# Performance work log

Measured on AMD Instinct MI355X. Metric: run time of the kernel, lower is better.

## Reference

```python
import jax, jax.numpy as jnp
import numpy as np

NUM_CLASSES = 19
EPS_MEAN = 1e-6   # torch: denominator eps in per-class mean
EPS_COS = 1e-8    # torch CosineSimilarity default eps


def _nearest_resize_labels(target, H, W):
    # torch nn.Upsample(mode='nearest'): in_idx = floor(out_idx * in / out)
    th, tw = target.shape[1], target.shape[2]
    ih = (jnp.arange(H) * th) // H
    iw = (jnp.arange(W) * tw) // W
    return target[:, ih][:, :, iw]  # [B,H,W]


def _class_centers(feat, lab):
    # feat: [B,C,H,W]; lab: [B,H,W] int. Single-pass segment mean by class,
    # then scatter means back to pixels whose label is in [0, NUM_CLASSES).
    B, C, H, W = feat.shape
    f = feat.reshape(B, C, H * W)                 # [B,C,N]
    l = lab.reshape(B, H * W)                      # [B,N]
    onehot = jax.nn.one_hot(l, NUM_CLASSES, dtype=feat.dtype)  # [B,N,K]; out-of-range -> all-zero row
    sums = jnp.einsum('bcn,bnk->bck', f, onehot)   # per-class channel sums
    counts = onehot.sum(axis=1)                    # [B,K]
    means = sums / (counts[:, None, :] + EPS_MEAN) # [B,C,K]
    gathered = jnp.einsum('bck,bnk->bcn', means, onehot)  # mean at each valid pixel, 0 elsewhere
    valid = (l >= 0) & (l < NUM_CLASSES)           # [B,N]
    center = jnp.where(valid[:, None, :], gathered, f)
    return center.reshape(B, C, H, W)


def _cosine_dim1(a, b):
    # torch CosineSimilarity(dim=1): dot / (max(||a||,eps) * max(||b||,eps))
    num = (a * b).sum(axis=1)
    na = jnp.sqrt((a * a).sum(axis=1))
    nb = jnp.sqrt((b * b).sum(axis=1))
    return num / (jnp.maximum(na, EPS_COS) * jnp.maximum(nb, EPS_COS))


def setup_inputs() -> dict:
    key = jax.random.key(0)
    k1, k2, k3 = jax.random.split(key, 3)
    B, C, H, W = 8, 512, 64, 64
    preds_S = jax.random.normal(k1, (B, C, H, W), dtype=jnp.float32)
    preds_T = jax.random.normal(k2, (B, C, H, W), dtype=jnp.float32)
    target = jax.random.randint(k3, (B, 512, 512), 0, NUM_CLASSES, dtype=jnp.int64)
    return {"preds_S": preds_S, "preds_T": preds_T, "target": target}


def reference(preds_S, preds_T, target):
    H, W = preds_S.shape[2], preds_S.shape[3]
    lab = _nearest_resize_labels(target, H, W)     # [B,H,W]
    center_S = _class_centers(preds_S, lab)
    center_T = _class_centers(preds_T, lab)
    pcsim_S = _cosine_dim1(preds_S, center_S)      # [B,H,W]
    pcsim_T = _cosine_dim1(preds_T, center_T)
    return jnp.mean((pcsim_S - pcsim_T) ** 2)
```

## Files before the change

kernel.cpp:

```cpp
#include <hip/hip_runtime.h>

#define NCLS   19
#define NB     8
#define NC     512
#define NHW    4096
#define EPSM   1e-6f
#define EPSC   1e-8f

#define OFF_LABELS   0u
#define OFF_COUNTS   131072u
#define OFF_SUMS_S   132096u
#define OFF_SUMS_T   443392u
#define OFF_NORM_S   754688u
#define OFF_NORM_T   755712u
#define OFF_PART     756736u

template<int CTRL>
__device__ __forceinline__ float dpp_add(float x) {
    int y = __builtin_amdgcn_update_dpp(0, __float_as_int(x), CTRL, 0xf, 0xf, false);
    return x + __int_as_float(y);
}
__device__ __forceinline__ float wave64_sum(float x) {
    x = dpp_add<0x111>(x);
    x = dpp_add<0x112>(x);
    x = dpp_add<0x114>(x);
    x = dpp_add<0x118>(x);
    x = dpp_add<0x142>(x);
    x = dpp_add<0x143>(x);
    return x;
}

__global__ __launch_bounds__(256) void k_labels(const int* __restrict__ target,
                                                int* __restrict__ labels,
                                                float* __restrict__ counts) {
    __shared__ int hist[NCLS];
    const int b = blockIdx.x;
    const int t = threadIdx.x;
    if (t < NCLS) hist[t] = 0;
    __syncthreads();
    const int* tb = target + (size_t)b * 512 * 512;
    #pragma unroll
    for (int i = 0; i < 16; ++i) {
        int n = t + i * 256;
        int y = n >> 6, x = n & 63;
        int l = tb[(y * 8) * 512 + x * 8];
        labels[b * NHW + n] = l;
        if (l >= 0 && l < NCLS) atomicAdd(&hist[l], 1);
    }
    __syncthreads();
    if (t < NCLS) counts[b * NCLS + t] = (float)hist[t];
}

__global__ __launch_bounds__(256, 2) void k_sums(const float* __restrict__ fS,
                                                 const float* __restrict__ fT,
                                                 const int* __restrict__ labels,
                                                 float* __restrict__ sumsS,
                                                 float* __restrict__ sumsT) {
    const int t = threadIdx.x;
    const int lane = t & 63;
    const int u = (blockIdx.x << 2) + (t >> 6);
    const int b = u >> 8;
    const int c0 = (u & 255) << 1;
    const size_t base = ((size_t)(b * NC) + c0) * NHW;
    const float4* pS0 = (const float4*)(fS + base);
    const float4* pS1 = (const float4*)(fS + base + NHW);
    const float4* pT0 = (const float4*)(fT + base);
    const float4* pT1 = (const float4*)(fT + base + NHW);
    const int4* lab4 = (const int4*)(labels + b * NHW);

    float aS0[NCLS], aS1[NCLS], aT0[NCLS], aT1[NCLS];
    #pragma unroll
    for (int k = 0; k < NCLS; ++k) { aS0[k] = aS1[k] = aT0[k] = aT1[k] = 0.f; }

    #pragma unroll 2
    for (int i = 0; i < 16; ++i) {
        const int idx = lane + (i << 6);
        const float4 vS0 = pS0[idx];
        const float4 vS1 = pS1[idx];
        const float4 vT0 = pT0[idx];
        const float4 vT1 = pT1[idx];
        const int4 l4 = lab4[idx];
        #pragma unroll
        for (int k = 0; k < NCLS; ++k) {
            const float m0 = (l4.x == k) ? 1.f : 0.f;
            const float m1 = (l4.y == k) ? 1.f : 0.f;
            const float m2 = (l4.z == k) ? 1.f : 0.f;
            const float m3 = (l4.w == k) ? 1.f : 0.f;
            aS0[k] += m0 * vS0.x + m1 * vS0.y + m2 * vS0.z + m3 * vS0.w;
            aS1[k] += m0 * vS1.x + m1 * vS1.y + m2 * vS1.z + m3 * vS1.w;
            aT0[k] += m0 * vT0.x + m1 * vT0.y + m2 * vT0.z + m3 * vT0.w;
            aT1[k] += m0 * vT1.x + m1 * vT1.y + m2 * vT1.z + m3 * vT1.w;
        }
    }
    #pragma unroll
    for (int k = 0; k < NCLS; ++k) {
        aS0[k] = wave64_sum(aS0[k]);
        aS1[k] = wave64_sum(aS1[k]);
        aT0[k] = wave64_sum(aT0[k]);
        aT1[k] = wave64_sum(aT1[k]);
    }
    if (lane == 63) {
        #pragma unroll
        for (int k = 0; k < NCLS; ++k) {
            float2* dS = (float2*)(sumsS + ((size_t)(b * NCLS + k)) * NC + c0);
            float2* dT = (float2*)(sumsT + ((size_t)(b * NCLS + k)) * NC + c0);
            *dS = make_float2(aS0[k], aS1[k]);
            *dT = make_float2(aT0[k], aT1[k]);
        }
    }
}

__global__ __launch_bounds__(64) void k_means(float* __restrict__ sumsS,
                                              float* __restrict__ sumsT,
                                              const float* __restrict__ counts,
                                              float* __restrict__ normS,
                                              float* __restrict__ normT) {
    const int bk = blockIdx.x;
    const int t = threadIdx.x;
    const float inv = 1.f / (counts[bk] + EPSM);
    float* rS = sumsS + (size_t)bk * NC;
    float* rT = sumsT + (size_t)bk * NC;
    float aS = 0.f, aT = 0.f;
    #pragma unroll
    for (int i = 0; i < NC / 64; ++i) {
        float mS = rS[t + i * 64] * inv; rS[t + i * 64] = mS; aS += mS * mS;
        float mT = rT[t + i * 64] * inv; rT[t + i * 64] = mT; aT += mT * mT;
    }
    aS = wave64_sum(aS);
    aT = wave64_sum(aT);
    if (t == 63) { normS[bk] = sqrtf(aS); normT[bk] = sqrtf(aT); }
}

#define CCH 64
__global__ __launch_bounds__(256) void k_dots(const float* __restrict__ fS,
                                              const float* __restrict__ fT,
                                              const float* __restrict__ meansS,
                                              const float* __restrict__ meansT,
                                              const int* __restrict__ labels,
                                              float* __restrict__ part) {
    __shared__ float mS[NCLS * 65];
    __shared__ float mT[NCLS * 65];
    const int blk = blockIdx.x;
    const int chunk = blk & 7;
    const int tile  = (blk >> 3) & 15;
    const int b     = blk >> 7;
    const int t = threadIdx.x;
    const int c0 = chunk * CCH;
    const int n = tile * 256 + t;

    for (int i = t; i < NCLS * CCH; i += 256) {
        const int k = i >> 6, j = i & 63;
        mS[k * 65 + j] = meansS[((size_t)(b * NCLS + k)) * NC + c0 + j];
        mT[k * 65 + j] = meansT[((size_t)(b * NCLS + k)) * NC + c0 + j];
    }
    __syncthreads();

    const int l = labels[b * NHW + n];
    const int lc = (l >= 0 && l < NCLS) ? l : 0;
    const float* pS = fS + ((size_t)(b * NC + c0)) * NHW + n;
    const float* pT = fT + ((size_t)(b * NC + c0)) * NHW + n;
    float dS = 0.f, nS = 0.f, dT = 0.f, nT = 0.f;
    #pragma unroll 8
    for (int ci = 0; ci < CCH; ++ci) {
        const float vS = pS[(size_t)ci * NHW];
        const float vT = pT[(size_t)ci * NHW];
        const float ms = mS[lc * 65 + ci];
        const float mt = mT[lc * 65 + ci];
        dS += vS * ms; nS += vS * vS;
        dT += vT * mt; nT += vT * vT;
    }
    const int p = b * NHW + n;
    part[((size_t)(0 * 8 + chunk)) * (NB * NHW) + p] = dS;
    part[((size_t)(1 * 8 + chunk)) * (NB * NHW) + p] = nS;
    part[((size_t)(2 * 8 + chunk)) * (NB * NHW) + p] = dT;
    part[((size_t)(3 * 8 + chunk)) * (NB * NHW) + p] = nT;
}

__global__ __launch_bounds__(256) void k_final(const float* __restrict__ part,
                                               const int* __restrict__ labels,
                                               const float* __restrict__ normS,
                                               const float* __restrict__ normT,
                                               float* __restrict__ out) {
    __shared__ float red[4];
    const int p = blockIdx.x * 256 + threadIdx.x;
    const int b = p >> 12;
    float dS = 0.f, nS = 0.f, dT = 0.f, nT = 0.f;
    #pragma unroll
    for (int ch = 0; ch < 8; ++ch) {
        dS += part[((size_t)(0 * 8 + ch)) * (NB * NHW) + p];
        nS += part[((size_t)(1 * 8 + ch)) * (NB * NHW) + p];
        dT += part[((size_t)(2 * 8 + ch)) * (NB * NHW) + p];
        nT += part[((size_t)(3 * 8 + ch)) * (NB * NHW) + p];
    }
    const int l = labels[p];
    float val = 0.f;
    if (l >= 0 && l < NCLS) {
        float cS = dS / (fmaxf(sqrtf(nS), EPSC) * fmaxf(normS[b * NCLS + l], EPSC));
        float cT = dT / (fmaxf(sqrtf(nT), EPSC) * fmaxf(normT[b * NCLS + l], EPSC));
        float d = cS - cT;
        val = d * d;
    }
    val = wave64_sum(val);
    if ((threadIdx.x & 63) == 63) red[threadIdx.x >> 6] = val;
    __syncthreads();
    if (threadIdx.x == 0)
        atomicAdd(out, (red[0] + red[1] + red[2] + red[3]) * (1.f / (NB * NHW)));
}

extern "C" void kernel_launch(void* const* d_in, const int* in_sizes, int n_in,
                              void* d_out, int out_size, void* d_ws, size_t ws_size,
                              hipStream_t stream) {
    (void)in_sizes; (void)n_in; (void)out_size; (void)ws_size;
    const float* fS     = (const float*)d_in[0];
    const float* fT     = (const float*)d_in[1];
    const int*   target = (const int*)d_in[2];

    char* ws = (char*)d_ws;
    int*   labels = (int*)  (ws + OFF_LABELS);
    float* counts = (float*)(ws + OFF_COUNTS);
    float* sumsS  = (float*)(ws + OFF_SUMS_S);
    float* sumsT  = (float*)(ws + OFF_SUMS_T);
    float* normS  = (float*)(ws + OFF_NORM_S);
    float* normT  = (float*)(ws + OFF_NORM_T);
    float* part   = (float*)(ws + OFF_PART);

    hipMemsetAsync(d_out, 0, sizeof(float), stream);

    k_labels<<<NB, 256, 0, stream>>>(target, labels, counts);
    k_sums  <<<NB * NC / 8, 256, 0, stream>>>(fS, fT, labels, sumsS, sumsT);
    k_means <<<NB * NCLS, 64, 0, stream>>>(sumsS, sumsT, counts, normS, normT);
    k_dots  <<<NB * 16 * 8, 256, 0, stream>>>(fS, fT, sumsS, sumsT, labels, part);
    k_final <<<NB * NHW / 256, 256, 0, stream>>>(part, labels, normS, normT,
                                                 (float*)d_out);
}
```

Before: 211.7 us.

## Split per-class sum reduction over pixel halves to double k_sums parallelism

The per-class channel-sum kernel now gives each wave only half of the pixel range and writes two partial-sum buffers. The means kernel adds the two partials before normalising. This doubles the block count and raises the launch-bounds occupancy hint, aiming to expose more memory-level parallelism in the bandwidth-heavy pass. The k_dots channel loop unroll also goes from 8 to 16. The cost is extra workspace and one more read of the partial sums, and the higher occupancy target may force register spills given the 76 accumulators per thread.

```diff
diff --git a/kernel.cpp b/kernel.cpp
--- a/kernel.cpp
+++ b/kernel.cpp
@@ -9,11 +9,13 @@
 
 #define OFF_LABELS   0u
 #define OFF_COUNTS   131072u
-#define OFF_SUMS_S   132096u
-#define OFF_SUMS_T   443392u
-#define OFF_NORM_S   754688u
-#define OFF_NORM_T   755712u
-#define OFF_PART     756736u
+#define OFF_SUMS_S0  132096u
+#define OFF_SUMS_S1  443392u
+#define OFF_SUMS_T0  754688u
+#define OFF_SUMS_T1  1065984u
+#define OFF_NORM_S   1377280u
+#define OFF_NORM_T   1378304u
+#define OFF_PART     1379328u
 
 template<int CTRL>
 __device__ __forceinline__ float dpp_add(float x) {
@@ -51,30 +53,35 @@
     if (t < NCLS) counts[b * NCLS + t] = (float)hist[t];
 }
 
-__global__ __launch_bounds__(256, 2) void k_sums(const float* __restrict__ fS,
+__global__ __launch_bounds__(256, 4) void k_sums(const float* __restrict__ fS,
                                                  const float* __restrict__ fT,
                                                  const int* __restrict__ labels,
-                                                 float* __restrict__ sumsS,
-                                                 float* __restrict__ sumsT) {
+                                                 float* __restrict__ psS0,
+                                                 float* __restrict__ psS1,
+                                                 float* __restrict__ psT0,
+                                                 float* __restrict__ psT1) {
     const int t = threadIdx.x;
     const int lane = t & 63;
     const int u = (blockIdx.x << 2) + (t >> 6);
-    const int b = u >> 8;
-    const int c0 = (u & 255) << 1;
+    const int b = u >> 9;
+    const int r = u & 511;
+    const int c0 = (r >> 1) << 1;
+    const int half = r & 1;
     const size_t base = ((size_t)(b * NC) + c0) * NHW;
     const float4* pS0 = (const float4*)(fS + base);
     const float4* pS1 = (const float4*)(fS + base + NHW);
     const float4* pT0 = (const float4*)(fT + base);
     const float4* pT1 = (const float4*)(fT + base + NHW);
     const int4* lab4 = (const int4*)(labels + b * NHW);
+    const int poff = half << 9;
 
     float aS0[NCLS], aS1[NCLS], aT0[NCLS], aT1[NCLS];
     #pragma unroll
     for (int k = 0; k < NCLS; ++k) { aS0[k] = aS1[k] = aT0[k] = aT1[k] = 0.f; }
 
     #pragma unroll 2
-    for (int i = 0; i < 16; ++i) {
-        const int idx = lane + (i << 6);
+    for (int i = 0; i < 8; ++i) {
+        const int idx = poff + lane + (i << 6);
         const float4 vS0 = pS0[idx];
         const float4 vS1 = pS1[idx];
         const float4 vT0 = pT0[idx];
@@ -100,31 +107,35 @@
         aT1[k] = wave64_sum(aT1[k]);
     }
     if (lane == 63) {
+        float* dS = half ? psS1 : psS0;
+        float* dT = half ? psT1 : psT0;
         #pragma unroll
         for (int k = 0; k < NCLS; ++k) {
-            float2* dS = (float2*)(sumsS + ((size_t)(b * NCLS + k)) * NC + c0);
-            float2* dT = (float2*)(sumsT + ((size_t)(b * NCLS + k)) * NC + c0);
-            *dS = make_float2(aS0[k], aS1[k]);
-            *dT = make_float2(aT0[k], aT1[k]);
+            *(float2*)(dS + ((size_t)(b * NCLS + k)) * NC + c0) = make_float2(aS0[k], aS1[k]);
+            *(float2*)(dT + ((size_t)(b * NCLS + k)) * NC + c0) = make_float2(aT0[k], aT1[k]);
         }
     }
 }
 
-__global__ __launch_bounds__(64) void k_means(float* __restrict__ sumsS,
-                                              float* __restrict__ sumsT,
+__global__ __launch_bounds__(64) void k_means(float* __restrict__ psS0,
+                                              const float* __restrict__ psS1,
+                                              float* __restrict__ psT0,
+                                              const float* __restrict__ psT1,
                                               const float* __restrict__ counts,
                                               float* __restrict__ normS,
                                               float* __restrict__ normT) {
     const int bk = blockIdx.x;
     const int t = threadIdx.x;
     const float inv = 1.f / (counts[bk] + EPSM);
-    float* rS = sumsS + (size_t)bk * NC;
-    float* rT = sumsT + (size_t)bk * NC;
+    const size_t row = (size_t)bk * NC;
     float aS = 0.f, aT = 0.f;
     #pragma unroll
     for (int i = 0; i < NC / 64; ++i) {
-        float mS = rS[t + i * 64] * inv; rS[t + i * 64] = mS; aS += mS * mS;
-        float mT = rT[t + i * 64] * inv; rT[t + i * 64] = mT; aT += mT * mT;
+        const int c = t + i * 64;
+        float mS = (psS0[row + c] + psS1[row + c]) * inv;
+        float mT = (psT0[row + c] + psT1[row + c]) * inv;
+        psS0[row + c] = mS; aS += mS * mS;
+        psT0[row + c] = mT; aT += mT * mT;
     }
     aS = wave64_sum(aS);
     aT = wave64_sum(aT);
@@ -160,7 +171,7 @@
     const float* pS = fS + ((size_t)(b * NC + c0)) * NHW + n;
     const float* pT = fT + ((size_t)(b * NC + c0)) * NHW + n;
     float dS = 0.f, nS = 0.f, dT = 0.f, nT = 0.f;
-    #pragma unroll 8
+    #pragma unroll 16
     for (int ci = 0; ci < CCH; ++ci) {
         const float vS = pS[(size_t)ci * NHW];
         const float vT = pT[(size_t)ci * NHW];
@@ -218,8 +229,10 @@
     char* ws = (char*)d_ws;
     int*   labels = (int*)  (ws + OFF_LABELS);
     float* counts = (float*)(ws + OFF_COUNTS);
-    float* sumsS  = (float*)(ws + OFF_SUMS_S);
-    float* sumsT  = (float*)(ws + OFF_SUMS_T);
+    float* psS0   = (float*)(ws + OFF_SUMS_S0);
+    float* psS1   = (float*)(ws + OFF_SUMS_S1);
+    float* psT0   = (float*)(ws + OFF_SUMS_T0);
+    float* psT1   = (float*)(ws + OFF_SUMS_T1);
     float* normS  = (float*)(ws + OFF_NORM_S);
     float* normT  = (float*)(ws + OFF_NORM_T);
     float* part   = (float*)(ws + OFF_PART);
@@ -227,9 +240,9 @@
     hipMemsetAsync(d_out, 0, sizeof(float), stream);
 
     k_labels<<<NB, 256, 0, stream>>>(target, labels, counts);
-    k_sums  <<<NB * NC / 8, 256, 0, stream>>>(fS, fT, labels, sumsS, sumsT);
-    k_means <<<NB * NCLS, 64, 0, stream>>>(sumsS, sumsT, counts, normS, normT);
-    k_dots  <<<NB * 16 * 8, 256, 0, stream>>>(fS, fT, sumsS, sumsT, labels, part);
+    k_sums  <<<NB * NC / 4, 256, 0, stream>>>(fS, fT, labels, psS0, psS1, psT0, psT1);
+    k_means <<<NB * NCLS, 64, 0, stream>>>(psS0, psS1, psT0, psT1, counts, normS, normT);
+    k_dots  <<<NB * 16 * 8, 256, 0, stream>>>(fS, fT, psS0, psT0, labels, part);
     k_final <<<NB * NHW / 256, 256, 0, stream>>>(part, labels, normS, normT,
                                                  (float*)d_out);
 }
```

Result: slower. 410.7 us (+94.0%).
